# Optimization experiments

Hardware: AMD Instinct MI355X
Metric: run time of the kernel (lower is better)

The kernel has to match this reference:

```python
import jax, jax.numpy as jnp
import numpy as np

NUM_HEADS = 16
NUM_KV_HEADS = 8
HEAD_DIM = 128
ROPE_THETA = 10000.0
SOFTCAP = 50.0


def rotate_half(x):
    x1, x2 = jnp.split(x, 2, axis=-1)
    return jnp.concatenate((-x2, x1), axis=-1)


def rope_cos_sin(seq_len):
    inv_freq = 1.0 / (ROPE_THETA ** (jnp.arange(0, HEAD_DIM, 2, dtype=jnp.float32) / HEAD_DIM))
    t = jnp.arange(seq_len, dtype=jnp.float32)
    freqs = t[:, None] * inv_freq[None, :]          # [S, D/2]
    emb = jnp.concatenate((freqs, freqs), axis=-1)  # [S, D]
    return jnp.cos(emb), jnp.sin(emb)


def setup_inputs() -> dict:
    key = jax.random.key(0)
    k1, k2, k3, k4, k5 = jax.random.split(key, 5)
    B, S, H = 2, 2048, 2048
    sc = 1.0 / np.sqrt(H)
    return {
        "hidden_states": jax.random.normal(k1, (B, S, H), dtype=jnp.float32),
        "Wq": jax.random.normal(k2, (H, NUM_HEADS * HEAD_DIM), dtype=jnp.float32) * sc,
        "Wk": jax.random.normal(k3, (H, NUM_KV_HEADS * HEAD_DIM), dtype=jnp.float32) * sc,
        "Wv": jax.random.normal(k4, (H, NUM_KV_HEADS * HEAD_DIM), dtype=jnp.float32) * sc,
        "Wo": jax.random.normal(k5, (NUM_HEADS * HEAD_DIM, H), dtype=jnp.float32) * sc,
    }


def reference(hidden_states, Wq, Wk, Wv, Wo):
    B, S, _ = hidden_states.shape
    groups = NUM_HEADS // NUM_KV_HEADS

    # projections -> [B, heads, S, D]
    q = (hidden_states @ Wq).reshape(B, S, NUM_HEADS, HEAD_DIM).transpose(0, 2, 1, 3)
    k = (hidden_states @ Wk).reshape(B, S, NUM_KV_HEADS, HEAD_DIM).transpose(0, 2, 1, 3)
    v = (hidden_states @ Wv).reshape(B, S, NUM_KV_HEADS, HEAD_DIM).transpose(0, 2, 1, 3)

    cos, sin = rope_cos_sin(S)  # [S, D], broadcast over (B, heads)
    q = q * cos + rotate_half(q) * sin
    k = k * cos + rotate_half(k) * sin

    # GQA: expand KV heads (repeat_interleave along head dim)
    k = jnp.repeat(k, groups, axis=1)
    v = jnp.repeat(v, groups, axis=1)

    scores = jnp.einsum('bhsd,bhtd->bhst', q, k) / np.sqrt(HEAD_DIM)
    scores = jnp.tanh(scores / SOFTCAP) * SOFTCAP  # Gemma logit softcapping
    weights = jax.nn.softmax(scores.astype(jnp.float32), axis=-1).astype(q.dtype)

    out = jnp.einsum('bhst,bhtd->bhsd', weights, v)
    out = out.transpose(0, 2, 1, 3).reshape(B, S, NUM_HEADS * HEAD_DIM)
    return out @ Wo
```

## Files before the change

kernel.cpp:

```cpp
#include <hip/hip_runtime.h>
#include <math.h>

typedef __bf16 bf16;
typedef __bf16 bf16x8 __attribute__((ext_vector_type(8)));
typedef __bf16 bf16x4 __attribute__((ext_vector_type(4)));
typedef float f32x2 __attribute__((ext_vector_type(2)));
typedef float f32x4 __attribute__((ext_vector_type(4)));
typedef float f32x16 __attribute__((ext_vector_type(16)));
typedef unsigned int uint;
typedef uint u32x4 __attribute__((ext_vector_type(4)));
typedef uint u32x2 __attribute__((ext_vector_type(2)));
typedef __bf16 bf16x8_a __attribute__((ext_vector_type(8), __may_alias__));
typedef uint u32x2_a __attribute__((ext_vector_type(2), __may_alias__));
typedef __bf16 bf16x4_a __attribute__((ext_vector_type(4), __may_alias__));
typedef __bf16 bf16_a __attribute__((__may_alias__));

constexpr int BATCH = 2;
constexpr int SEQ   = 2048;
constexpr int HID   = 2048;
constexpr int NHEAD = 16;
constexpr int NKV   = 8;
constexpr int HD    = 128;
constexpr int MROWS = BATCH * SEQ;

#define DEVINL __device__ __forceinline__

#define BAR()                                 \
  do {                                        \
    asm volatile("" ::: "memory");            \
    __builtin_amdgcn_s_barrier();             \
    asm volatile("" ::: "memory");            \
  } while (0)

#define WAITV(N) asm volatile("s_waitcnt vmcnt(" #N ")" ::: "memory")

DEVINL void async16(void* l, const void* g) {
  __builtin_amdgcn_global_load_lds((const __attribute__((address_space(1))) void*)g,
                                   (__attribute__((address_space(3))) void*)l, 16, 0, 0);
}

DEVINL f32x4 mfma16(bf16x8 a, bf16x8 b, f32x4 c) {
  return __builtin_amdgcn_mfma_f32_16x16x32_bf16(a, b, c, 0, 0, 0);
}
DEVINL f32x16 mfma32(bf16x8 a, bf16x8 b, f32x16 c) {
  return __builtin_amdgcn_mfma_f32_32x32x16_bf16(a, b, c, 0, 0, 0);
}

DEVINL f32x4 fzero4() { f32x4 z; z[0] = 0.f; z[1] = 0.f; z[2] = 0.f; z[3] = 0.f; return z; }

DEVINL float ex2(float x) {
#if __has_builtin(__builtin_amdgcn_exp2f)
  return __builtin_amdgcn_exp2f(x);
#else
  return __expf(x * 0.6931471805599453f);
#endif
}

DEVINL uint pkbf16(float lo, float hi) {
  unsigned short l = __builtin_bit_cast(unsigned short, (bf16)lo);
  unsigned short h = __builtin_bit_cast(unsigned short, (bf16)hi);
  return (uint)l | ((uint)h << 16);
}

DEVINL u32x2 pswap(uint a, uint b) {
#if __has_builtin(__builtin_amdgcn_permlane32_swap)
  return __builtin_amdgcn_permlane32_swap(a, b, false, false);
#else
  int hl = (int)((threadIdx.x >> 5) & 1);
  uint as = __shfl_xor(a, 32), bs = __shfl_xor(b, 32);
  u32x2 r;
  r[0] = hl ? bs : a;
  r[1] = hl ? b : as;
  return r;
#endif
}

__global__ __launch_bounds__(256) void prep(const float* __restrict__ X,
                                            const float* __restrict__ Wq,
                                            const float* __restrict__ Wk,
                                            const float* __restrict__ Wv,
                                            const float* __restrict__ Wo,
                                            bf16* __restrict__ Xb,
                                            bf16* __restrict__ WqT, bf16* __restrict__ WkT,
                                            bf16* __restrict__ WvT, bf16* __restrict__ WoT,
                                            float* __restrict__ ct, float* __restrict__ st) {
  const int tid = threadIdx.x;
  const int z = blockIdx.z;
  if (z == 4) {
    int idx = (blockIdx.y * 32 + blockIdx.x) * 256 + tid;
    if (idx < SEQ * 64) {
      int s = idx >> 6, d = idx & 63;
      float freq = powf(10000.0f, -(float)d * (1.0f / 64.0f));
      float a = (float)s * freq;
      ct[idx] = cosf(a);
      st[idx] = sinf(a);
    }
    return;
  }
  if (z == 5) {
    int j = (blockIdx.y * 32 + blockIdx.x) * 256 + tid;
#pragma unroll
    for (int it = 0; it < 8; it++) {
      int e = (it * 262144 + j) * 4;
      float4 v = *(const float4*)(X + e);
      bf16x4 o;
      o[0] = (bf16)v.x; o[1] = (bf16)v.y; o[2] = (bf16)v.z; o[3] = (bf16)v.w;
      *(bf16x4*)(Xb + e) = o;
    }
    return;
  }
  __shared__ bf16 t[64][65];
  const float* W; bf16* WT; int N;
  switch (z) {
    case 0: W = Wq; WT = WqT; N = 2048; break;
    case 1: W = Wk; WT = WkT; N = 1024; break;
    case 2: W = Wv; WT = WvT; N = 1024; break;
    default: W = Wo; WT = WoT; N = 2048; break;
  }
  int n0 = blockIdx.x * 64, k0 = blockIdx.y * 64;
  if (n0 >= N) return;
#pragma unroll
  for (int p = 0; p < 4; p++) {
    int r = (tid >> 4) + p * 16;
    int c4 = (tid & 15) * 4;
    float4 v = *(const float4*)(&W[(size_t)(k0 + r) * N + n0 + c4]);
    t[r][c4 + 0] = (bf16)v.x;
    t[r][c4 + 1] = (bf16)v.y;
    t[r][c4 + 2] = (bf16)v.z;
    t[r][c4 + 3] = (bf16)v.w;
  }
  __syncthreads();
#pragma unroll
  for (int p = 0; p < 4; p++) {
    int nr = (tid >> 4) + p * 16;
    int kb = (tid & 15) * 4;
    bf16x4 o;
    o[0] = t[kb + 0][nr];
    o[1] = t[kb + 1][nr];
    o[2] = t[kb + 2][nr];
    o[3] = t[kb + 3][nr];
    *(bf16x4_a*)(&WT[(size_t)(n0 + nr) * 2048 + k0 + kb]) = o;
  }
}

__global__ __launch_bounds__(256) void vtrans(const bf16* __restrict__ V, bf16* __restrict__ VT) {
  __shared__ bf16 t[64][65];
  int s0 = blockIdx.x * 64, d0 = blockIdx.y * 64;
  int bh = blockIdx.z, b = bh >> 3, kvh = bh & 7;
  for (int i = threadIdx.x; i < 4096; i += 256) {
    int r = i >> 6, c = i & 63;
    t[r][c] = V[(size_t)(b * SEQ + s0 + r) * (NKV * HD) + kvh * HD + d0 + c];
  }
  __syncthreads();
  for (int i = threadIdx.x; i < 4096; i += 256) {
    int r = i >> 6, c = i & 63;
    VT[((size_t)bh * HD + d0 + r) * SEQ + s0 + c] = t[c][r];
  }
}

template <int EPI>
__global__ __launch_bounds__(512, 2) void gemm8p(const bf16* __restrict__ A,
                                                 const bf16* __restrict__ BT,
                                                 void* __restrict__ C0, void* __restrict__ C1,
                                                 void* __restrict__ C2, int M, int N, int K,
                                                 const float* __restrict__ ct,
                                                 const float* __restrict__ st) {
  __shared__ alignas(16) char ldsA[65536];
  __shared__ alignas(16) char ldsB[65536];
  const int tid = threadIdx.x, lane = tid & 63, w = tid >> 6;
  const int l15 = lane & 15, l4 = lane >> 4;
  const int wm = w >> 2, wn = w & 3;
  const int gx = gridDim.x;
  const int nwg = gx * gridDim.y;
  int id = blockIdx.y * gx + blockIdx.x;
  id = (id & 7) * (nwg >> 3) + (id >> 3);
  const int row0 = (id / gx) * 256;
  const int col0 = (id % gx) * 256;

  f32x4 acc[8][4];
#pragma unroll
  for (int mt = 0; mt < 8; mt++)
#pragma unroll
    for (int nt = 0; nt < 4; nt++) acc[mt][nt] = fzero4();

  const int rG0 = tid >> 3, sG0 = ((tid & 7) ^ (rG0 & 7)) * 8;
  const int ci1 = 512 + tid;
  const int rG1 = ci1 >> 3, sG1 = ((ci1 & 7) ^ (rG1 & 7)) * 8;
  const int dst0 = tid * 16, dst1 = (512 + tid) * 16;

  const bf16* Asrc = A + (size_t)row0 * K;
  const bf16* Bsrc = BT + (size_t)col0 * K;
  const int nk = K >> 6;

#define STG_A(half, kt, buf)                                         \
  {                                                                  \
    char* d = ldsA + (buf) * 32768 + (half) * 16384;                 \
    const bf16* s = Asrc + (size_t)((half) * 128) * K + (kt) * 64;   \
    async16(d + dst0, s + (size_t)rG0 * K + sG0);                    \
    async16(d + dst1, s + (size_t)rG1 * K + sG1);                    \
  }
#define STG_B(half, kt, buf)                                         \
  {                                                                  \
    char* d = ldsB + (buf) * 32768 + (half) * 16384;                 \
    const bf16* s = Bsrc + (size_t)((half) * 128) * K + (kt) * 64;   \
    async16(d + dst0, s + (size_t)rG0 * K + sG0);                    \
    async16(d + dst1, s + (size_t)rG1 * K + sG1);                    \
  }

  STG_A(0, 0, 0) STG_A(1, 0, 0) STG_B(0, 0, 0) STG_B(1, 0, 0)
  STG_B(0, 1, 1) STG_B(1, 1, 1) STG_A(0, 1, 1) STG_A(1, 1, 1)
  WAITV(8);
  BAR();

  bf16x8 af[8];
  bf16x8 bfr[2][4];

  for (int t = 0; t < nk; ++t) {
    const int buf = t & 1;
    const char* bA = ldsA + buf * 32768 + wm * 16384;
    const char* bB = ldsB + buf * 32768;
    const bool s2 = (t + 2) < nk;

#pragma unroll
    for (int mtp = 0; mtp < 4; mtp++)
#pragma unroll
      for (int kc = 0; kc < 2; kc++) {
        int r = mtp * 16 + l15;
        int off = ((r << 7) + ((kc * 4 + l4) << 4)) ^ ((r & 7) << 4);
        af[mtp * 2 + kc] = *(const bf16x8_a*)(bA + off);
      }
#pragma unroll
    for (int ntp = 0; ntp < 2; ntp++)
#pragma unroll
      for (int kc = 0; kc < 2; kc++) {
        int c = wn * 16 + ntp * 64 + l15;
        int off = ((c << 7) + ((kc * 4 + l4) << 4)) ^ ((c & 7) << 4);
        bfr[0][ntp * 2 + kc] = *(const bf16x8_a*)(bB + off);
      }
    BAR();
    __builtin_amdgcn_s_setprio(1);
#pragma unroll
    for (int mtp = 0; mtp < 4; mtp++)
#pragma unroll
      for (int ntp = 0; ntp < 2; ntp++)
#pragma unroll
        for (int kc = 0; kc < 2; kc++)
          acc[mtp][ntp] = mfma16(af[mtp * 2 + kc], bfr[0][ntp * 2 + kc], acc[mtp][ntp]);
    __builtin_amdgcn_s_setprio(0);
    BAR();

#pragma unroll
    for (int ntp = 0; ntp < 2; ntp++)
#pragma unroll
      for (int kc = 0; kc < 2; kc++) {
        int c = wn * 16 + ntp * 64 + l15;
        int off = 16384 + (((c << 7) + ((kc * 4 + l4) << 4)) ^ ((c & 7) << 4));
        bfr[1][ntp * 2 + kc] = *(const bf16x8_a*)(bB + off);
      }
    if (s2) STG_B(0, t + 2, buf)
    BAR();
    __builtin_amdgcn_s_setprio(1);
#pragma unroll
    for (int mtp = 0; mtp < 4; mtp++)
#pragma unroll
      for (int ntp = 0; ntp < 2; ntp++)
#pragma unroll
        for (int kc = 0; kc < 2; kc++)
          acc[mtp][ntp + 2] = mfma16(af[mtp * 2 + kc], bfr[1][ntp * 2 + kc], acc[mtp][ntp + 2]);
    __builtin_amdgcn_s_setprio(0);
    BAR();

#pragma unroll
    for (int mtp = 0; mtp < 4; mtp++)
#pragma unroll
      for (int kc = 0; kc < 2; kc++) {
        int r = 64 + mtp * 16 + l15;
        int off = ((r << 7) + ((kc * 4 + l4) << 4)) ^ ((r & 7) << 4);
        af[mtp * 2 + kc] = *(const bf16x8_a*)(bA + off);
      }
    if (s2) STG_B(1, t + 2, buf)
    BAR();
    __builtin_amdgcn_s_setprio(1);
#pragma unroll
    for (int mtp = 0; mtp < 4; mtp++)
#pragma unroll
      for (int ntp = 0; ntp < 2; ntp++)
#pragma unroll
        for (int kc = 0; kc < 2; kc++)
          acc[mtp + 4][ntp + 2] = mfma16(af[mtp * 2 + kc], bfr[1][ntp * 2 + kc], acc[mtp + 4][ntp + 2]);
    __builtin_amdgcn_s_setprio(0);
    BAR();

    if (s2) { STG_A(0, t + 2, buf) STG_A(1, t + 2, buf) }
    BAR();
    __builtin_amdgcn_s_setprio(1);
#pragma unroll
    for (int mtp = 0; mtp < 4; mtp++)
#pragma unroll
      for (int ntp = 0; ntp < 2; ntp++)
#pragma unroll
        for (int kc = 0; kc < 2; kc++)
          acc[mtp + 4][ntp] = mfma16(af[mtp * 2 + kc], bfr[0][ntp * 2 + kc], acc[mtp + 4][ntp]);
    __builtin_amdgcn_s_setprio(0);
    if (s2) { WAITV(8); } else { WAITV(0); }
    BAR();
  }
#undef STG_A
#undef STG_B

#pragma unroll
  for (int mt = 0; mt < 8; mt++)
#pragma unroll
    for (int nt = 0; nt < 4; nt++)
#pragma unroll
      for (int rg = 0; rg < 4; rg++) {
        int row = row0 + wm * 128 + mt * 16 + l4 * 4 + rg;
        int cl = col0 + wn * 16 + nt * 64 + l15;
        float v = acc[mt][nt][rg];
        if (EPI == 2) {
          ((float*)C0)[(size_t)row * N + cl] = v;
        } else {
          if (cl < 3072) {
            int s = row & (SEQ - 1);
            float cc = ct[s * 64 + wn * 16 + l15];
            float ss = st[s * 64 + wn * 16 + l15];
            float pv = acc[mt][nt ^ 1][rg];
            v = (nt & 1) ? fmaf(v, cc, pv * ss) : fmaf(v, cc, -pv * ss);
          }
          if (cl < 2048) {
            v *= 1.7677669529663689e-3f;
            ((bf16*)C0)[(size_t)row * 2048 + cl] = (bf16)v;
          } else if (cl < 3072) {
            ((bf16*)C1)[(size_t)row * 1024 + (cl - 2048)] = (bf16)v;
          } else {
            ((bf16*)C2)[(size_t)row * 1024 + (cl - 3072)] = (bf16)v;
          }
        }
      }
}

__global__ __launch_bounds__(512, 2) void gemm2p(const bf16* __restrict__ A,
                                                 const bf16* __restrict__ BT,
                                                 float* __restrict__ C, int M, int N, int K) {
  __shared__ alignas(16) char ldsA[65536];
  __shared__ alignas(16) char ldsB[49152];
  const int tid = threadIdx.x, lane = tid & 63, w = tid >> 6;
  const int l15 = lane & 15, l4 = lane >> 4;
  const int wm = w >> 1, wn = w & 1;
  const int gx = gridDim.x;
  const int nwg = gx * gridDim.y;
  int id = blockIdx.y * gx + blockIdx.x;
  id = (id & 7) * (nwg >> 3) + (id >> 3);
  const int row0 = (id / gx) * 256;
  const int col0 = (id % gx) * 128;

  f32x4 acc[4][4];
#pragma unroll
  for (int mt = 0; mt < 4; mt++)
#pragma unroll
    for (int nt = 0; nt < 4; nt++) acc[mt][nt] = fzero4();

  const int rG0 = tid >> 3, sG0 = ((tid & 7) ^ (rG0 & 7)) * 8;
  const int ci1 = 512 + tid;
  const int rG1 = ci1 >> 3, sG1 = ((ci1 & 7) ^ (rG1 & 7)) * 8;
  const int dst0 = tid * 16, dst1 = (512 + tid) * 16;

  const bf16* Asrc = A + (size_t)row0 * K;
  const bf16* Bsrc = BT + (size_t)col0 * K;
  const int nk = K >> 6;

#define STG_A2(half, kt, buf)                                        \
  {                                                                  \
    char* d = ldsA + (buf) * 32768 + (half) * 16384;                 \
    const bf16* s = Asrc + (size_t)((half) * 128) * K + (kt) * 64;   \
    async16(d + dst0, s + (size_t)rG0 * K + sG0);                    \
    async16(d + dst1, s + (size_t)rG1 * K + sG1);                    \
  }
#define STG_B2(kt, buf)                                              \
  {                                                                  \
    char* d = ldsB + (buf) * 16384;                                  \
    const bf16* s = Bsrc + (kt) * 64;                                \
    async16(d + dst0, s + (size_t)rG0 * K + sG0);                    \
    async16(d + dst1, s + (size_t)rG1 * K + sG1);                    \
  }

  STG_B2(0, 0) STG_A2(0, 0, 0) STG_A2(1, 0, 0)
  STG_B2(1, 1) STG_A2(0, 1, 1) STG_A2(1, 1, 1)
  WAITV(6);
  BAR();

  bf16x8 af[8];
  bf16x8 bfr[8];

  for (int t = 0; t < nk; ++t) {
    const int abuf = t & 1;
    int bb = t % 3;
    const char* bA = ldsA + abuf * 32768 + (wm >> 1) * 16384;
    const char* bB = ldsB + bb * 16384;
    const bool s2 = (t + 2) < nk;
    int bb2 = bb + 2; if (bb2 >= 3) bb2 -= 3;

#pragma unroll
    for (int mt = 0; mt < 4; mt++)
#pragma unroll
      for (int kc = 0; kc < 2; kc++) {
        int r = (wm & 1) * 64 + mt * 16 + l15;
        int off = ((r << 7) + ((kc * 4 + l4) << 4)) ^ ((r & 7) << 4);
        af[mt * 2 + kc] = *(const bf16x8_a*)(bA + off);
      }
#pragma unroll
    for (int nt = 0; nt < 2; nt++)
#pragma unroll
      for (int kc = 0; kc < 2; kc++) {
        int c = wn * 16 + nt * 32 + l15;
        int off = ((c << 7) + ((kc * 4 + l4) << 4)) ^ ((c & 7) << 4);
        bfr[nt * 2 + kc] = *(const bf16x8_a*)(bB + off);
      }
    if (s2) STG_B2(t + 2, bb2)
    BAR();
    __builtin_amdgcn_s_setprio(1);
#pragma unroll
    for (int mt = 0; mt < 4; mt++)
#pragma unroll
      for (int nt = 0; nt < 2; nt++)
#pragma unroll
        for (int kc = 0; kc < 2; kc++)
          acc[mt][nt] = mfma16(af[mt * 2 + kc], bfr[nt * 2 + kc], acc[mt][nt]);
    __builtin_amdgcn_s_setprio(0);
    BAR();

#pragma unroll
    for (int nt = 0; nt < 2; nt++)
#pragma unroll
      for (int kc = 0; kc < 2; kc++) {
        int c = wn * 16 + (nt + 2) * 32 + l15;
        int off = ((c << 7) + ((kc * 4 + l4) << 4)) ^ ((c & 7) << 4);
        bfr[4 + nt * 2 + kc] = *(const bf16x8_a*)(bB + off);
      }
    if (s2) { STG_A2(0, t + 2, abuf) STG_A2(1, t + 2, abuf) }
    BAR();
    __builtin_amdgcn_s_setprio(1);
#pragma unroll
    for (int mt = 0; mt < 4; mt++)
#pragma unroll
      for (int nt = 0; nt < 2; nt++)
#pragma unroll
        for (int kc = 0; kc < 2; kc++)
          acc[mt][nt + 2] = mfma16(af[mt * 2 + kc], bfr[4 + nt * 2 + kc], acc[mt][nt + 2]);
    __builtin_amdgcn_s_setprio(0);
    if (s2) { WAITV(6); } else { WAITV(0); }
    BAR();
  }
#undef STG_A2
#undef STG_B2

#pragma unroll
  for (int mt = 0; mt < 4; mt++)
#pragma unroll
    for (int nt = 0; nt < 4; nt++)
#pragma unroll
      for (int rg = 0; rg < 4; rg++) {
        int row = row0 + wm * 64 + mt * 16 + l4 * 4 + rg;
        int cl = col0 + wn * 16 + nt * 32 + l15;
        C[(size_t)row * N + cl] = acc[mt][nt][rg];
      }
}

__global__ __launch_bounds__(512, 2) void attn10(const bf16* __restrict__ Q,
                                                 const bf16* __restrict__ Kg,
                                                 const bf16* __restrict__ VTg,
                                                 bf16* __restrict__ O) {
  __shared__ alignas(16) char ldsK[49152];
  __shared__ alignas(16) char ldsV[49152];
  const int tid = threadIdx.x, lane = tid & 63, w = tid >> 6;
  const int l31 = lane & 31, hl = lane >> 5;

  const int nx = gridDim.x, ny = gridDim.y;
  const int nwg = nx * ny * gridDim.z;
  int id = (blockIdx.z * ny + blockIdx.y) * nx + blockIdx.x;
  id = (id & 7) * (nwg >> 3) + (id >> 3);
  const int qt = id % nx; id /= nx;
  const int h = id % ny; const int b = id / ny;
  const int kvh = h >> 1;
  const int qrow = b * SEQ + qt * 256 + w * 32 + l31;

  bf16x8 qf[8];
  const bf16* qp = Q + (size_t)qrow * (NHEAD * HD) + h * HD + hl * 8;
#pragma unroll
  for (int kc = 0; kc < 8; kc++) qf[kc] = *(const bf16x8_a*)(qp + kc * 16);

  f32x16 oT[4];
#pragma unroll
  for (int dt = 0; dt < 4; dt++)
#pragma unroll
    for (int r = 0; r < 16; r++) oT[dt][r] = 0.f;
  f32x2 ls2; ls2[0] = 0.f; ls2[1] = 0.f;

  const int rK = tid >> 4, sK = (tid & 15) ^ (rK & 15);
  const int rV = tid >> 3, sV = (tid & 7) ^ (rV & 7);
  const size_t koff0 = (size_t)(b * SEQ + rK) * (NKV * HD) + kvh * HD + sK * 8;
  const size_t voff0 = ((size_t)(b * NKV + kvh) * HD + rV) * SEQ + sV * 8;

  const float Ac = 72.13475204444817f;
  const float Bc = -24.044917348149389f;

  auto STAGE = [&](int buf, int t) {
    char* dK = ldsK + buf * 16384;
    char* dV = ldsV + buf * 16384;
    const bf16* ks = Kg + koff0 + (size_t)t * (64 * NKV * HD);
    const bf16* vs = VTg + voff0 + (size_t)t * 64;
    async16(dK + tid * 16, ks);
    async16(dK + (512 + tid) * 16, ks + (size_t)32 * (NKV * HD));
    async16(dV + tid * 16, vs);
    async16(dV + (512 + tid) * 16, vs + (size_t)64 * SEQ);
  };

  const int kvr0 = l31, kvr1 = 32 + l31;

#define QKT(SC, lKp)                                                     \
  do {                                                                   \
    _Pragma("unroll")                                                    \
    for (int r = 0; r < 16; r++) { (SC)[0][r] = 0.f; (SC)[1][r] = 0.f; } \
    _Pragma("unroll")                                                    \
    for (int kc = 0; kc < 8; kc++) {                                     \
      int slot = kc * 2 + hl;                                            \
      int off0 = (kvr0 << 8) | ((slot ^ (kvr0 & 15)) << 4);              \
      int off1 = (kvr1 << 8) | ((slot ^ (kvr1 & 15)) << 4);              \
      bf16x8 kf0 = *(const bf16x8_a*)((lKp) + off0);                     \
      bf16x8 kf1 = *(const bf16x8_a*)((lKp) + off1);                     \
      (SC)[0] = mfma32(kf0, qf[kc], (SC)[0]);                            \
      (SC)[1] = mfma32(kf1, qf[kc], (SC)[1]);                            \
    }                                                                    \
  } while (0)

#define SOFTMAX(SC, PB)                                                  \
  do {                                                                   \
    _Pragma("unroll")                                                    \
    for (int ntb = 0; ntb < 2; ntb++) {                                  \
      uint u[4][2];                                                      \
      _Pragma("unroll")                                                  \
      for (int r2 = 0; r2 < 8; r2++) {                                   \
        f32x2 z; z[0] = (SC)[ntb][2 * r2]; z[1] = (SC)[ntb][2 * r2 + 1]; \
        f32x2 z2 = z * z;                                                \
        f32x2 wv = z2 * Bc + Ac;                                         \
        f32x2 e = z * wv;                                                \
        float p0 = ex2(e[0]), p1 = ex2(e[1]);                            \
        ls2[0] += p0; ls2[1] += p1;                                      \
        u[r2 >> 1][r2 & 1] = pkbf16(p0, p1);                             \
      }                                                                  \
      _Pragma("unroll")                                                  \
      for (int sub = 0; sub < 2; sub++) {                                \
        u32x2 r0 = pswap(u[2 * sub][0], u[2 * sub + 1][0]);              \
        u32x2 r1 = pswap(u[2 * sub][1], u[2 * sub + 1][1]);              \
        u32x4 bu;                                                        \
        bu[0] = r0[0];                                                   \
        bu[1] = r1[0];                                                   \
        bu[2] = r0[1];                                                   \
        bu[3] = r1[1];                                                   \
        (PB)[ntb * 2 + sub] = __builtin_bit_cast(bf16x8, bu);            \
      }                                                                  \
    }                                                                    \
  } while (0)

#define PVACC(PB, lVp)                                                   \
  do {                                                                   \
    _Pragma("unroll")                                                    \
    for (int kvb = 0; kvb < 4; kvb++) {                                  \
      int slot = kvb * 2 + hl;                                           \
      _Pragma("unroll")                                                  \
      for (int dt = 0; dt < 4; dt++) {                                   \
        int d = dt * 32 + l31;                                           \
        int off = (d << 7) | ((slot ^ (d & 7)) << 4);                    \
        bf16x8 vf = *(const bf16x8_a*)((lVp) + off);                     \
        oT[dt] = mfma32(vf, (PB)[kvb], oT[dt]);                          \
      }                                                                  \
    }                                                                    \
  } while (0)

  constexpr int NT = SEQ / 64;
  STAGE(0, 0);
  STAGE(1, 1);
  WAITV(4);
  BAR();

  f32x16 scA[2], scB[2];
  bf16x8 pb[4];
  QKT(scA, ldsK);

  for (int it = 0; it < NT / 2; ++it) {
    const int t0 = 2 * it;
    {
      const int t = t0;
      BAR();
      if (t + 2 < NT) STAGE((t + 2) % 3, t + 2);
      SOFTMAX(scA, pb);
      if (t + 2 < NT) { WAITV(4); } else { WAITV(0); }
      BAR();
      __builtin_amdgcn_s_setprio(1);
      if (t + 1 < NT) QKT(scB, ldsK + ((t + 1) % 3) * 16384);
      PVACC(pb, ldsV + (t % 3) * 16384);
      __builtin_amdgcn_s_setprio(0);
    }
    {
      const int t = t0 + 1;
      BAR();
      if (t + 2 < NT) STAGE((t + 2) % 3, t + 2);
      SOFTMAX(scB, pb);
      if (t + 2 < NT) { WAITV(4); } else { WAITV(0); }
      BAR();
      __builtin_amdgcn_s_setprio(1);
      if (t + 1 < NT) QKT(scA, ldsK + ((t + 1) % 3) * 16384);
      PVACC(pb, ldsV + (t % 3) * 16384);
      __builtin_amdgcn_s_setprio(0);
    }
  }
#undef QKT
#undef SOFTMAX
#undef PVACC

  float lsum = ls2[0] + ls2[1];
  float lsf = lsum + __shfl_xor(lsum, 32);
  float inv = 1.0f / lsf;
  bf16* ob = O + (size_t)qrow * (NHEAD * HD) + h * HD;
#pragma unroll
  for (int dt = 0; dt < 4; dt++)
#pragma unroll
    for (int g = 0; g < 4; g++) {
      u32x2 pr;
      pr[0] = pkbf16(oT[dt][4 * g] * inv, oT[dt][4 * g + 1] * inv);
      pr[1] = pkbf16(oT[dt][4 * g + 2] * inv, oT[dt][4 * g + 3] * inv);
      *(u32x2_a*)(ob + dt * 32 + 8 * g + 4 * hl) = pr;
    }
}

extern "C" void kernel_launch(void* const* d_in, const int* in_sizes, int n_in,
                              void* d_out, int out_size, void* d_ws, size_t ws_size,
                              hipStream_t stream) {
  const float* X  = (const float*)d_in[0];
  const float* Wq = (const float*)d_in[1];
  const float* Wk = (const float*)d_in[2];
  const float* Wv = (const float*)d_in[3];
  const float* Wo = (const float*)d_in[4];
  float* out = (float*)d_out;

  char* ws = (char*)d_ws;
  size_t off = 0;
  auto alloc = [&](size_t bytes) {
    void* p = ws + off;
    off += (bytes + 255) & ~(size_t)255;
    return p;
  };
  bf16* Xb  = (bf16*)alloc((size_t)MROWS * HID * 2);
  bf16* WqT = (bf16*)alloc((size_t)2048 * 2048 * 2);
  bf16* WkT = (bf16*)alloc((size_t)1024 * 2048 * 2);
  bf16* WvT = (bf16*)alloc((size_t)1024 * 2048 * 2);
  bf16* WoT = (bf16*)alloc((size_t)2048 * 2048 * 2);
  bf16* Qb  = (bf16*)alloc((size_t)MROWS * 2048 * 2);
  bf16* Kb  = (bf16*)alloc((size_t)MROWS * 1024 * 2);
  bf16* Vb  = (bf16*)alloc((size_t)MROWS * 1024 * 2);
  bf16* VTb = (bf16*)alloc((size_t)16 * 128 * 2048 * 2);
  bf16* AOb = (bf16*)alloc((size_t)MROWS * 2048 * 2);
  float* ct = (float*)alloc((size_t)SEQ * 64 * 4);
  float* st = (float*)alloc((size_t)SEQ * 64 * 4);

  prep<<<dim3(32, 32, 6), 256, 0, stream>>>(X, Wq, Wk, Wv, Wo, Xb, WqT, WkT, WvT, WoT, ct, st);
  gemm8p<1><<<dim3(16, 16), 512, 0, stream>>>(Xb, WqT, Qb, Kb, Vb, MROWS, 4096, 2048, ct, st);
  vtrans<<<dim3(32, 2, 16), 256, 0, stream>>>(Vb, VTb);
  attn10<<<dim3(8, 16, 2), 512, 0, stream>>>(Qb, Kb, VTb, AOb);
  gemm2p<<<dim3(16, 16), 512, 0, stream>>>(AOb, WoT, out, MROWS, 2048, 2048);

  (void)in_sizes; (void)n_in; (void)out_size; (void)ws_size;
}
```

Before: 235.4 us.

## Merge GEMM k-step phases to cut barriers and issue prefetches earlier

Both projection GEMM main loops now read all B fragments from LDS in one pass. The fused-QKV kernel goes from four MFMA phases per k-step to two, and the output GEMM goes from two phases to one. Global-to-LDS prefetch stores for step t+2 are issued together, right after the first barrier. The aim is fewer workgroup barriers and longer uninterrupted MFMA runs. In exchange, more B fragments are held in registers at once, which raises register pressure and may lower occupancy. The epilogue column formula is rewritten but computes the same columns.

```diff
diff --git a/kernel.cpp b/kernel.cpp
--- a/kernel.cpp
+++ b/kernel.cpp
@@ -236,37 +236,21 @@
         int c = wn * 16 + ntp * 64 + l15;
         int off = ((c << 7) + ((kc * 4 + l4) << 4)) ^ ((c & 7) << 4);
         bfr[0][ntp * 2 + kc] = *(const bf16x8_a*)(bB + off);
+        bfr[1][ntp * 2 + kc] = *(const bf16x8_a*)(bB + 16384 + off);
       }
     BAR();
+    if (s2) { STG_B(0, t + 2, buf) STG_B(1, t + 2, buf) }
     __builtin_amdgcn_s_setprio(1);
 #pragma unroll
     for (int mtp = 0; mtp < 4; mtp++)
 #pragma unroll
-      for (int ntp = 0; ntp < 2; ntp++)
-#pragma unroll
-        for (int kc = 0; kc < 2; kc++)
-          acc[mtp][ntp] = mfma16(af[mtp * 2 + kc], bfr[0][ntp * 2 + kc], acc[mtp][ntp]);
-    __builtin_amdgcn_s_setprio(0);
-    BAR();
-
-#pragma unroll
-    for (int ntp = 0; ntp < 2; ntp++)
-#pragma unroll
-      for (int kc = 0; kc < 2; kc++) {
-        int c = wn * 16 + ntp * 64 + l15;
-        int off = 16384 + (((c << 7) + ((kc * 4 + l4) << 4)) ^ ((c & 7) << 4));
-        bfr[1][ntp * 2 + kc] = *(const bf16x8_a*)(bB + off);
-      }
-    if (s2) STG_B(0, t + 2, buf)
-    BAR();
-    __builtin_amdgcn_s_setprio(1);
-#pragma unroll
-    for (int mtp = 0; mtp < 4; mtp++)
-#pragma unroll
-      for (int ntp = 0; ntp < 2; ntp++)
-#pragma unroll
-        for (int kc = 0; kc < 2; kc++)
-          acc[mtp][ntp + 2] = mfma16(af[mtp * 2 + kc], bfr[1][ntp * 2 + kc], acc[mtp][ntp + 2]);
+      for (int half = 0; half < 2; half++)
+#pragma unroll
+        for (int ntp = 0; ntp < 2; ntp++)
+#pragma unroll
+          for (int kc = 0; kc < 2; kc++)
+            acc[mtp][half * 2 + ntp] =
+                mfma16(af[mtp * 2 + kc], bfr[half][ntp * 2 + kc], acc[mtp][half * 2 + ntp]);
     __builtin_amdgcn_s_setprio(0);
     BAR();
 
@@ -278,29 +262,19 @@
         int off = ((r << 7) + ((kc * 4 + l4) << 4)) ^ ((r & 7) << 4);
         af[mtp * 2 + kc] = *(const bf16x8_a*)(bA + off);
       }
-    if (s2) STG_B(1, t + 2, buf)
     BAR();
+    if (s2) { STG_A(0, t + 2, buf) STG_A(1, t + 2, buf) }
     __builtin_amdgcn_s_setprio(1);
 #pragma unroll
     for (int mtp = 0; mtp < 4; mtp++)
 #pragma unroll
-      for (int ntp = 0; ntp < 2; ntp++)
-#pragma unroll
-        for (int kc = 0; kc < 2; kc++)
-          acc[mtp + 4][ntp + 2] = mfma16(af[mtp * 2 + kc], bfr[1][ntp * 2 + kc], acc[mtp + 4][ntp + 2]);
-    __builtin_amdgcn_s_setprio(0);
-    BAR();
-
-    if (s2) { STG_A(0, t + 2, buf) STG_A(1, t + 2, buf) }
-    BAR();
-    __builtin_amdgcn_s_setprio(1);
-#pragma unroll
-    for (int mtp = 0; mtp < 4; mtp++)
-#pragma unroll
-      for (int ntp = 0; ntp < 2; ntp++)
-#pragma unroll
-        for (int kc = 0; kc < 2; kc++)
-          acc[mtp + 4][ntp] = mfma16(af[mtp * 2 + kc], bfr[0][ntp * 2 + kc], acc[mtp + 4][ntp]);
+      for (int half = 0; half < 2; half++)
+#pragma unroll
+        for (int ntp = 0; ntp < 2; ntp++)
+#pragma unroll
+          for (int kc = 0; kc < 2; kc++)
+            acc[mtp + 4][half * 2 + ntp] =
+                mfma16(af[mtp * 2 + kc], bfr[half][ntp * 2 + kc], acc[mtp + 4][half * 2 + ntp]);
     __builtin_amdgcn_s_setprio(0);
     if (s2) { WAITV(8); } else { WAITV(0); }
     BAR();
@@ -315,8 +289,11 @@
 #pragma unroll
       for (int rg = 0; rg < 4; rg++) {
         int row = row0 + wm * 128 + mt * 16 + l4 * 4 + rg;
-        int cl = col0 + wn * 16 + nt * 64 + l15;
+        int ntL = (nt & 1) + (nt >> 1) * 2;
+        int cl = col0 + wn * 16 + ((nt >> 1) * 128) + ((nt & 1) * 64);
+        (void)ntL;
         float v = acc[mt][nt][rg];
+        cl += l15;
         if (EPI == 2) {
           ((float*)C0)[(size_t)row * N + cl] = v;
         } else {
@@ -409,44 +386,23 @@
         af[mt * 2 + kc] = *(const bf16x8_a*)(bA + off);
       }
 #pragma unroll
-    for (int nt = 0; nt < 2; nt++)
+    for (int nt = 0; nt < 4; nt++)
 #pragma unroll
       for (int kc = 0; kc < 2; kc++) {
         int c = wn * 16 + nt * 32 + l15;
         int off = ((c << 7) + ((kc * 4 + l4) << 4)) ^ ((c & 7) << 4);
         bfr[nt * 2 + kc] = *(const bf16x8_a*)(bB + off);
       }
-    if (s2) STG_B2(t + 2, bb2)
     BAR();
+    if (s2) { STG_B2(t + 2, bb2) STG_A2(0, t + 2, abuf) STG_A2(1, t + 2, abuf) }
     __builtin_amdgcn_s_setprio(1);
 #pragma unroll
     for (int mt = 0; mt < 4; mt++)
 #pragma unroll
-      for (int nt = 0; nt < 2; nt++)
+      for (int nt = 0; nt < 4; nt++)
 #pragma unroll
         for (int kc = 0; kc < 2; kc++)
           acc[mt][nt] = mfma16(af[mt * 2 + kc], bfr[nt * 2 + kc], acc[mt][nt]);
-    __builtin_amdgcn_s_setprio(0);
-    BAR();
-
-#pragma unroll
-    for (int nt = 0; nt < 2; nt++)
-#pragma unroll
-      for (int kc = 0; kc < 2; kc++) {
-        int c = wn * 16 + (nt + 2) * 32 + l15;
-        int off = ((c << 7) + ((kc * 4 + l4) << 4)) ^ ((c & 7) << 4);
-        bfr[4 + nt * 2 + kc] = *(const bf16x8_a*)(bB + off);
-      }
-    if (s2) { STG_A2(0, t + 2, abuf) STG_A2(1, t + 2, abuf) }
-    BAR();
-    __builtin_amdgcn_s_setprio(1);
-#pragma unroll
-    for (int mt = 0; mt < 4; mt++)
-#pragma unroll
-      for (int nt = 0; nt < 2; nt++)
-#pragma unroll
-        for (int kc = 0; kc < 2; kc++)
-          acc[mt][nt + 2] = mfma16(af[mt * 2 + kc], bfr[4 + nt * 2 + kc], acc[mt][nt + 2]);
     __builtin_amdgcn_s_setprio(0);
     if (s2) { WAITV(6); } else { WAITV(0); }
     BAR();
```

Measured after the change: 235.6 us. Within noise of the previous version (+0.1%).
